# Performance work log

Measured on AMD Instinct MI355X. Metric: run time of the kernel, lower is better.

## Reference

```python
import jax, jax.numpy as jnp
import numpy as np

NUM_HEADS = 12
DIM_HEAD = 64
EPS = 1e-5


def _layer_norm(x, g, b):
    m = jnp.mean(x, axis=-1, keepdims=True)
    v = jnp.mean(jnp.square(x - m), axis=-1, keepdims=True)
    return (x - m) * jax.lax.rsqrt(v + EPS) * g + b


def setup_inputs() -> dict:
    key = jax.random.key(0)
    ks = jax.random.split(key, 3)
    B, S, L, D = 1, 128, 256, NUM_HEADS * DIM_HEAD
    x = jax.random.normal(ks[0], (B, S, L, D), dtype=jnp.float32)
    w_row = jax.random.normal(ks[1], (3 * D, D), dtype=jnp.float32) * 0.02
    b_row = jnp.zeros((3 * D,), dtype=jnp.float32)
    w_col = jax.random.normal(ks[2], (3 * D, D), dtype=jnp.float32) * 0.02
    b_col = jnp.zeros((3 * D,), dtype=jnp.float32)
    g1 = jnp.ones((D,), dtype=jnp.float32)
    beta1 = jnp.zeros((D,), dtype=jnp.float32)
    g2 = jnp.ones((D,), dtype=jnp.float32)
    beta2 = jnp.zeros((D,), dtype=jnp.float32)
    return {"x": x, "w_row": w_row, "b_row": b_row, "w_col": w_col,
            "b_col": b_col, "g1": g1, "beta1": beta1, "g2": g2, "beta2": beta2}


def reference(x, w_row, b_row, w_col, b_col, g1, beta1, g2, beta2):
    B, S, L, D = x.shape
    H, dh = NUM_HEADS, DIM_HEAD

    def qkv(inp, w, b):
        p = inp @ w.T + b                      # [B,S,L,3D]
        q, k, v = jnp.split(p, 3, axis=-1)
        rs = lambda t: t.reshape(B, S, L, H, dh)
        return rs(q), rs(k), rs(v)

    # --- tied row attention: logits summed over S (no 1/sqrt(dh) scaling, as in source) ---
    q, k, v = qkv(x, w_row, b_row)
    row_attn = jnp.einsum('bsihc,bsjhc->bhij', q, k)      # [B,H,L,L]
    row_attn = jax.nn.softmax(row_attn, axis=-1)
    row_out = jnp.einsum('bhij,bsjhd->bsihd', row_attn, v).reshape(B, S, L, D)
    out = _layer_norm(x + row_out, g1, beta1)

    # --- column attention: softmax over the j (sequence) axis ---
    q, k, v = qkv(out, w_col, b_col)
    col_attn = jnp.einsum('bilhc,bjlhc->bhijl', q, k)     # [B,H,S,S,L]
    col_attn = jax.nn.softmax(col_attn, axis=-2)
    col_out = jnp.einsum('bhijl,bjlhd->bilhd', col_attn, v).reshape(B, S, L, D)
    out = _layer_norm(out + col_out, g2, beta2)
    return out
```

## Files before the change

### kernel.cpp

```cpp
#include <hip/hip_runtime.h>

#define S_DIM 128
#define L_DIM 256
#define D_DIM 768
#define H_DIM 12
#define TD    2304
#define NROW  32768
#define KDIM  768
#define LN_EPS 1e-5f

typedef unsigned short u16;
typedef unsigned int   u32;
typedef _Float16 f16;
typedef _Float16 f16x8 __attribute__((ext_vector_type(8)));
typedef _Float16 f16x4 __attribute__((ext_vector_type(4)));
typedef float    f32x4 __attribute__((ext_vector_type(4)));

#define WS_QT_OFF     0
#define WS_KT_OFF     50331648
#define WS_VT_OFF     100663296
#define WS_P_OFF      0
#define WS_LPART_OFF  150994944
#define WS_PT_OFF     163577856
#define WS_XH_OFF     166723584
#define WS_WRH_OFF    217055232
#define WS_WCH_OFF    220594176

__device__ __forceinline__ float h2f(u16 v) {
    union { u16 u; f16 h; } c; c.u = v; return (float)c.h;
}

__device__ __forceinline__ void gload_lds16(const void* g, void* l) {
    __builtin_amdgcn_global_load_lds((const __attribute__((address_space(1))) void*)g,
                                     (__attribute__((address_space(3))) void*)l, 16, 0, 0);
}

__global__ __launch_bounds__(256)
void cvt_f32_f16(const float* __restrict__ in, f16* __restrict__ out)
{
    int i = blockIdx.x * 256 + threadIdx.x;
    float4 v = ((const float4*)in)[i];
    f16x4 o; o.x = (f16)v.x; o.y = (f16)v.y; o.z = (f16)v.z; o.w = (f16)v.w;
    ((f16x4*)out)[i] = o;
}

#define MFMA_PROLOG(KROW)                                                     \
    __shared__ f16 As[128 * 32];                                              \
    __shared__ f16 Bs[128 * 32];                                              \
    const int tid  = threadIdx.x;                                             \
    const int lane = tid & 63;                                                \
    const int w    = tid >> 6;                                                \
    const int wr   = (w >> 1) * 64;                                           \
    const int wc   = (w & 1) * 64;                                            \
    const int lm   = lane & 15;                                               \
    const int q    = lane >> 4;                                               \
    size_t soff[2];                                                           \
    int    ldsc[2];                                                           \
    _Pragma("unroll")                                                         \
    for (int t = 0; t < 2; ++t) {                                             \
        int c  = w * 128 + t * 64 + lane;                                     \
        int m  = c >> 2;                                                      \
        int gj = (c & 3) ^ ((m >> 1) & 3);                                    \
        soff[t] = (size_t)m * (KROW) + gj * 8;                                \
        ldsc[t] = (w * 128 + t * 64) * 8;                                     \
    }                                                                         \
    int chA[4], chB[4];                                                       \
    _Pragma("unroll")                                                         \
    for (int t = 0; t < 4; ++t) {                                             \
        int ma = wr + t * 16 + lm;                                            \
        chA[t] = ma * 4 + (q ^ ((ma >> 1) & 3));                              \
        int mb = wc + t * 16 + lm;                                            \
        chB[t] = mb * 4 + (q ^ ((mb >> 1) & 3));                              \
    }                                                                         \
    f32x4 acc[4][4];                                                          \
    _Pragma("unroll")                                                         \
    for (int i = 0; i < 4; ++i)                                               \
        _Pragma("unroll")                                                     \
        for (int j = 0; j < 4; ++j) acc[i][j] = (f32x4)0.f;

#define MFMA_KLOOP(baseA, baseB, KLEN)                                        \
    for (int k0 = 0; k0 < (KLEN); k0 += 32) {                                 \
        _Pragma("unroll")                                                     \
        for (int t = 0; t < 2; ++t) {                                         \
            gload_lds16((baseA) + soff[t] + k0, &As[ldsc[t]]);                \
            gload_lds16((baseB) + soff[t] + k0, &Bs[ldsc[t]]);                \
        }                                                                     \
        __syncthreads();                                                      \
        f16x8 af[4], bf[4];                                                   \
        _Pragma("unroll")                                                     \
        for (int t = 0; t < 4; ++t) af[t] = *(const f16x8*)&As[chA[t] * 8];   \
        _Pragma("unroll")                                                     \
        for (int t = 0; t < 4; ++t) bf[t] = *(const f16x8*)&Bs[chB[t] * 8];   \
        _Pragma("unroll")                                                     \
        for (int mt = 0; mt < 4; ++mt)                                        \
            _Pragma("unroll")                                                 \
            for (int nt = 0; nt < 4; ++nt)                                    \
                acc[mt][nt] = __builtin_amdgcn_mfma_f32_16x16x32_f16(         \
                    af[mt], bf[nt], acc[mt][nt], 0, 0, 0);                    \
        __syncthreads();                                                      \
    }

__global__ __launch_bounds__(256)
void mfma_gemm_qkv(const f16* __restrict__ A, const f16* __restrict__ W,
                   const float* __restrict__ bias, f16* __restrict__ C)
{
    const int row0 = blockIdx.y * 128;
    const int col0 = blockIdx.x * 128;
    MFMA_PROLOG(KDIM)
    const f16* baseA = A + (size_t)row0 * KDIM;
    const f16* baseB = W + (size_t)col0 * KDIM;
    MFMA_KLOOP(baseA, baseB, KDIM)

    float bv[4];
#pragma unroll
    for (int nt = 0; nt < 4; ++nt) bv[nt] = bias[col0 + wc + nt * 16 + lm];
#pragma unroll
    for (int mt = 0; mt < 4; ++mt) {
        int grow = row0 + wr + mt * 16 + q * 4;
#pragma unroll
        for (int nt = 0; nt < 4; ++nt) {
            int gcol = col0 + wc + nt * 16 + lm;
#pragma unroll
            for (int r = 0; r < 4; ++r)
                C[(size_t)(grow + r) * TD + gcol] = (f16)(acc[mt][nt][r] + bv[nt]);
        }
    }
}

__global__ __launch_bounds__(256)
void mfma_gemm_row(const f16* __restrict__ A, const f16* __restrict__ W,
                   const float* __restrict__ bias,
                   f16* __restrict__ qt, f16* __restrict__ kt,
                   f16* __restrict__ vt)
{
    const int row0 = blockIdx.y * 128;
    const int col0 = blockIdx.x * 128;
    MFMA_PROLOG(KDIM)
    const f16* baseA = A + (size_t)row0 * KDIM;
    const f16* baseB = W + (size_t)col0 * KDIM;
    MFMA_KLOOP(baseA, baseB, KDIM)

    if (col0 < 1536) {
        f16* dst = (col0 < 768) ? qt : kt;
        const int cbase = (col0 < 768) ? col0 : col0 - 768;
#pragma unroll
        for (int nt = 0; nt < 4; ++nt) {
            int gcol = cbase + wc + nt * 16 + lm;
            int h = gcol >> 6, c = gcol & 63;
            float b = bias[col0 + wc + nt * 16 + lm];
#pragma unroll
            for (int mt = 0; mt < 4; ++mt) {
                int n0 = row0 + wr + mt * 16 + q * 4;
#pragma unroll
                for (int r = 0; r < 4; ++r) {
                    int n = n0 + r;
                    int s = n >> 8, i = n & 255;
                    dst[(((size_t)h * 256 + i) * 128 + s) * 64 + c] =
                        (f16)(acc[mt][nt][r] + b);
                }
            }
        }
    } else {
#pragma unroll
        for (int nt = 0; nt < 4; ++nt) {
            int gcol = col0 + wc + nt * 16 + lm;
            int vcol = gcol - 1536;
            int h = vcol >> 6, d = vcol & 63;
            float b = bias[gcol];
#pragma unroll
            for (int mt = 0; mt < 4; ++mt) {
                int n0 = row0 + wr + mt * 16 + q * 4;
                int s = n0 >> 8, j0 = n0 & 255;
                f16x4 pack;
#pragma unroll
                for (int r = 0; r < 4; ++r) pack[r] = (f16)(acc[mt][nt][r] + b);
                *(f16x4*)&vt[((((size_t)h * 128 + s) * 64 + d) << 8) + j0] = pack;
            }
        }
    }
}

__global__ __launch_bounds__(256)
void row_logits_mfma(const f16* __restrict__ qt, const f16* __restrict__ kt,
                     float* __restrict__ lpart)
{
    const int i0 = blockIdx.y * 128;
    const int j0 = blockIdx.x * 128;
    const int h  = blockIdx.z >> 2;
    const int sp = blockIdx.z & 3;
    MFMA_PROLOG(8192)
    const f16* baseA = qt + ((size_t)h * 256 + i0) * 8192 + sp * 2048;
    const f16* baseB = kt + ((size_t)h * 256 + j0) * 8192 + sp * 2048;
    MFMA_KLOOP(baseA, baseB, 2048)

    float* outp = lpart + (size_t)(sp * 12 + h) * 65536;
#pragma unroll
    for (int mt = 0; mt < 4; ++mt) {
        int grow = i0 + wr + mt * 16 + q * 4;
#pragma unroll
        for (int nt = 0; nt < 4; ++nt) {
            int gcol = j0 + wc + nt * 16 + lm;
#pragma unroll
            for (int r = 0; r < 4; ++r)
                outp[(size_t)(grow + r) * 256 + gcol] = acc[mt][nt][r];
        }
    }
}

__global__ __launch_bounds__(256)
void softmax256_4(const float* __restrict__ lpart, f16* __restrict__ pt)
{
    __shared__ float red[256];
    const int t = threadIdx.x;
    const size_t idx = (size_t)blockIdx.x * 256 + t;
    const size_t P = (size_t)12 * 65536;
    float v = lpart[idx] + lpart[idx + P] + lpart[idx + 2*P] + lpart[idx + 3*P];
    red[t] = v; __syncthreads();
    for (int w = 128; w > 0; w >>= 1) { if (t < w) red[t] = fmaxf(red[t], red[t+w]); __syncthreads(); }
    float m = red[0];
    __syncthreads();
    float e = __expf(v - m);
    red[t] = e; __syncthreads();
    for (int w = 128; w > 0; w >>= 1) { if (t < w) red[t] += red[t+w]; __syncthreads(); }
    pt[idx] = (f16)(e / red[0]);
}

__global__ __launch_bounds__(256)
void row_pv_mfma(const f16* __restrict__ pt, const f16* __restrict__ vt,
                 float* __restrict__ rout)
{
    const int n0t = blockIdx.x * 128;
    const int i0  = blockIdx.y * 128;
    const int h   = blockIdx.z;
    MFMA_PROLOG(256)
    const f16* baseA = pt + (size_t)h * 65536 + (size_t)i0 * 256;
    const f16* baseB = vt + ((size_t)h * 8192 + n0t) * 256;
    MFMA_KLOOP(baseA, baseB, 256)

#pragma unroll
    for (int mt = 0; mt < 4; ++mt) {
        int irow = i0 + wr + mt * 16 + q * 4;
#pragma unroll
        for (int nt = 0; nt < 4; ++nt) {
            int n = n0t + wc + nt * 16 + lm;
            int s = n >> 6, d = n & 63;
#pragma unroll
            for (int r = 0; r < 4; ++r)
                rout[(size_t)(s * 256 + irow + r) * D_DIM + h * 64 + d] =
                    acc[mt][nt][r];
        }
    }
}

__global__ __launch_bounds__(256)
void add_ln_out16(const float* __restrict__ x, const float* __restrict__ r,
                  const float* __restrict__ g, const float* __restrict__ beta,
                  f16* __restrict__ out16)
{
    __shared__ float red[256];
    const int n = blockIdx.x, t = threadIdx.x;
    const float* xp = x + (size_t)n * D_DIM;
    const float* rp = r + (size_t)n * D_DIM;
    float v[3]; float s = 0.f;
#pragma unroll
    for (int e = 0; e < 3; ++e) { v[e] = xp[t + e*256] + rp[t + e*256]; s += v[e]; }
    red[t] = s; __syncthreads();
    for (int w = 128; w > 0; w >>= 1) { if (t < w) red[t] += red[t+w]; __syncthreads(); }
    float mean = red[0] * (1.f/768.f);
    __syncthreads();
    float sq = 0.f;
#pragma unroll
    for (int e = 0; e < 3; ++e) { float d = v[e] - mean; sq += d*d; }
    red[t] = sq; __syncthreads();
    for (int w = 128; w > 0; w >>= 1) { if (t < w) red[t] += red[t+w]; __syncthreads(); }
    float rstd = rsqrtf(red[0] * (1.f/768.f) + LN_EPS);
#pragma unroll
    for (int e = 0; e < 3; ++e) {
        int idx = t + e*256;
        out16[(size_t)n * D_DIM + idx] = (f16)((v[e] - mean) * rstd * g[idx] + beta[idx]);
    }
}

__global__ __launch_bounds__(256)
void add_ln_in16(const f16* __restrict__ x16, float* __restrict__ r,
                 const float* __restrict__ g, const float* __restrict__ beta)
{
    __shared__ float red[256];
    const int n = blockIdx.x, t = threadIdx.x;
    const f16*   xp = x16 + (size_t)n * D_DIM;
    float*       rp = r   + (size_t)n * D_DIM;
    float v[3]; float s = 0.f;
#pragma unroll
    for (int e = 0; e < 3; ++e) { v[e] = (float)xp[t + e*256] + rp[t + e*256]; s += v[e]; }
    red[t] = s; __syncthreads();
    for (int w = 128; w > 0; w >>= 1) { if (t < w) red[t] += red[t+w]; __syncthreads(); }
    float mean = red[0] * (1.f/768.f);
    __syncthreads();
    float sq = 0.f;
#pragma unroll
    for (int e = 0; e < 3; ++e) { float d = v[e] - mean; sq += d*d; }
    red[t] = sq; __syncthreads();
    for (int w = 128; w > 0; w >>= 1) { if (t < w) red[t] += red[t+w]; __syncthreads(); }
    float rstd = rsqrtf(red[0] * (1.f/768.f) + LN_EPS);
#pragma unroll
    for (int e = 0; e < 3; ++e) {
        int idx = t + e*256;
        rp[idx] = (v[e] - mean) * rstd * g[idx] + beta[idx];
    }
}

__global__ __launch_bounds__(256, 3)
void col_attn_mfma(const f16* __restrict__ p, float* __restrict__ cout)
{
    __shared__ char smem[54272];
    f16* Qs = (f16*)smem;
    f16* Ks = (f16*)(smem + 18432);
    f16* Ps = (f16*)smem;
    f16* Vt = (f16*)(smem + 36864);

    const int tid  = threadIdx.x;
    const int lane = tid & 63;
    const int w    = tid >> 6;
    const int lm   = lane & 15;
    const int q    = lane >> 4;
    const int l = blockIdx.x, h = blockIdx.y;
    const int ib = w * 32;

    {
        const int r  = tid >> 1;
        const int hc = (tid & 1) * 32;
        const f16* rowp = p + (size_t)(r * 256 + l) * TD + h * 64 + hc;
#pragma unroll
        for (int cc = 0; cc < 4; ++cc)
            *(float4*)&Qs[r * 72 + hc + cc * 8] = *(const float4*)(rowp + cc * 8);
#pragma unroll
        for (int cc = 0; cc < 4; ++cc)
            *(float4*)&Ks[r * 72 + hc + cc * 8] = *(const float4*)(rowp + 768 + cc * 8);
#pragma unroll
        for (int cc = 0; cc < 4; ++cc) {
            union { float4 f; u16 u[8]; } vb;
            vb.f = *(const float4*)(rowp + 1536 + cc * 8);
#pragma unroll
            for (int e = 0; e < 8; ++e) {
                int d = hc + cc * 8 + e;
                ((u16*)Vt)[d * 136 + r] = vb.u[e];
            }
        }
    }
    __syncthreads();

    f32x4 acc[2][8];
#pragma unroll
    for (int mt = 0; mt < 2; ++mt)
#pragma unroll
        for (int nt = 0; nt < 8; ++nt) acc[mt][nt] = (f32x4)0.f;
#pragma unroll
    for (int ks = 0; ks < 2; ++ks) {
        f16x8 af[2];
#pragma unroll
        for (int mt = 0; mt < 2; ++mt)
            af[mt] = *(const f16x8*)&Qs[(ib + mt * 16 + lm) * 72 + ks * 32 + q * 8];
#pragma unroll
        for (int nt = 0; nt < 8; ++nt) {
            f16x8 bf = *(const f16x8*)&Ks[(nt * 16 + lm) * 72 + ks * 32 + q * 8];
#pragma unroll
            for (int mt = 0; mt < 2; ++mt)
                acc[mt][nt] = __builtin_amdgcn_mfma_f32_16x16x32_f16(
                    af[mt], bf, acc[mt][nt], 0, 0, 0);
        }
    }
    __syncthreads();

    float inv_sum[2][4];
#pragma unroll
    for (int mt = 0; mt < 2; ++mt) {
#pragma unroll
        for (int r = 0; r < 4; ++r) {
            float m = acc[mt][0][r];
#pragma unroll
            for (int nt = 1; nt < 8; ++nt) m = fmaxf(m, acc[mt][nt][r]);
#pragma unroll
            for (int d = 1; d < 16; d <<= 1) m = fmaxf(m, __shfl_xor(m, d));
            float s = 0.f;
#pragma unroll
            for (int nt = 0; nt < 8; ++nt) {
                float e = __expf(acc[mt][nt][r] - m);
                acc[mt][nt][r] = e; s += e;
            }
#pragma unroll
            for (int d = 1; d < 16; d <<= 1) s += __shfl_xor(s, d);
            inv_sum[mt][r] = 1.f / s;
        }
        const int irow = ib + mt * 16 + q * 4;
#pragma unroll
        for (int nt = 0; nt < 8; ++nt) {
            const int jj = nt * 16 + lm;
#pragma unroll
            for (int r = 0; r < 4; ++r)
                Ps[(irow + r) * 136 + jj] = (f16)acc[mt][nt][r];
        }
    }
    __syncthreads();

    f32x4 acc2[2][4];
#pragma unroll
    for (int mt = 0; mt < 2; ++mt)
#pragma unroll
        for (int nt = 0; nt < 4; ++nt) acc2[mt][nt] = (f32x4)0.f;
#pragma unroll
    for (int ks = 0; ks < 4; ++ks) {
        f16x8 pf[2];
#pragma unroll
        for (int mt = 0; mt < 2; ++mt)
            pf[mt] = *(const f16x8*)&Ps[(ib + mt * 16 + lm) * 136 + ks * 32 + q * 8];
#pragma unroll
        for (int nt = 0; nt < 4; ++nt) {
            f16x8 vf = *(const f16x8*)&Vt[(nt * 16 + lm) * 136 + ks * 32 + q * 8];
#pragma unroll
            for (int mt = 0; mt < 2; ++mt)
                acc2[mt][nt] = __builtin_amdgcn_mfma_f32_16x16x32_f16(
                    pf[mt], vf, acc2[mt][nt], 0, 0, 0);
        }
    }

#pragma unroll
    for (int mt = 0; mt < 2; ++mt) {
        const int irow = ib + mt * 16 + q * 4;
#pragma unroll
        for (int nt = 0; nt < 4; ++nt) {
            const int d = nt * 16 + lm;
#pragma unroll
            for (int r = 0; r < 4; ++r)
                cout[(size_t)((irow + r) * 256 + l) * D_DIM + h * 64 + d] =
                    acc2[mt][nt][r] * inv_sum[mt][r];
        }
    }
}

extern "C" void kernel_launch(void* const* d_in, const int* in_sizes, int n_in,
                              void* d_out, int out_size, void* d_ws, size_t ws_size,
                              hipStream_t stream)
{
    const float* x     = (const float*)d_in[0];
    const float* w_row = (const float*)d_in[1];
    const float* b_row = (const float*)d_in[2];
    const float* w_col = (const float*)d_in[3];
    const float* b_col = (const float*)d_in[4];
    const float* g1    = (const float*)d_in[5];
    const float* be1   = (const float*)d_in[6];
    const float* g2    = (const float*)d_in[7];
    const float* be2   = (const float*)d_in[8];
    float* out = (float*)d_out;

    char* ws = (char*)d_ws;
    f16*   qt     = (f16*)(ws + WS_QT_OFF);
    f16*   kt     = (f16*)(ws + WS_KT_OFF);
    f16*   vt     = (f16*)(ws + WS_VT_OFF);
    f16*   p      = (f16*)(ws + WS_P_OFF);
    float* lpart  = (float*)(ws + WS_LPART_OFF);
    f16*   pt     = (f16*)(ws + WS_PT_OFF);
    f16*   xh     = (f16*)(ws + WS_XH_OFF);
    f16*   wrh    = (f16*)(ws + WS_WRH_OFF);
    f16*   wch    = (f16*)(ws + WS_WCH_OFF);

    cvt_f32_f16<<<NROW * D_DIM / 1024, 256, 0, stream>>>(x, xh);
    cvt_f32_f16<<<TD * D_DIM / 1024, 256, 0, stream>>>(w_row, wrh);
    cvt_f32_f16<<<TD * D_DIM / 1024, 256, 0, stream>>>(w_col, wch);
    mfma_gemm_row<<<dim3(TD/128, NROW/128), 256, 0, stream>>>(xh, wrh, b_row, qt, kt, vt);
    row_logits_mfma<<<dim3(2, 2, 48), 256, 0, stream>>>(qt, kt, lpart);
    softmax256_4<<<H_DIM * L_DIM, 256, 0, stream>>>(lpart, pt);
    row_pv_mfma<<<dim3(64, 2, H_DIM), 256, 0, stream>>>(pt, vt, out);
    add_ln_out16<<<NROW, 256, 0, stream>>>(x, out, g1, be1, xh);
    mfma_gemm_qkv<<<dim3(TD/128, NROW/128), 256, 0, stream>>>(xh, wch, b_col, p);
    col_attn_mfma<<<dim3(L_DIM, H_DIM), 256, 0, stream>>>(p, out);
    add_ln_in16<<<NROW, 256, 0, stream>>>(xh, out, g2, be2);
}
```

Measured before the change: 737.4 us.

## Use 256x256 double-buffered MFMA tiles with XOR LDS swizzle and grid remap for QKV GEMMs

Replaces the 128x128 single-buffered GEMM tile with a 256x256 tile computed by 512 threads. The K loop uses two LDS buffers so the next K slice loads while the current one computes. LDS reads use an XOR-swizzled layout, and the block index is remapped so neighbouring blocks share A and B tiles in cache. s_setprio is raised around the MFMA bursts. The aim is higher operand reuse, fewer bank conflicts and hidden load latency in the two large projection GEMMs. The cost is higher register and LDS use (128KB of LDS per block), which may limit occupancy.

```diff
diff --git a/kernel.cpp b/kernel.cpp
--- a/kernel.cpp
+++ b/kernel.cpp
@@ -100,22 +100,101 @@
         __syncthreads();                                                      \
     }
 
-__global__ __launch_bounds__(256)
+#define G256_PROLOG(KROW)                                                     \
+    __shared__ f16 As0[256 * 64];                                             \
+    __shared__ f16 Bs0[256 * 64];                                             \
+    __shared__ f16 As1[256 * 64];                                             \
+    __shared__ f16 Bs1[256 * 64];                                             \
+    const int tid  = threadIdx.x;                                             \
+    const int lane = tid & 63;                                                \
+    const int w    = tid >> 6;                                                \
+    const int wr   = (w >> 2) * 128;                                          \
+    const int wc   = (w & 3) * 64;                                            \
+    const int lm   = lane & 15;                                               \
+    const int q    = lane >> 4;                                               \
+    size_t soff[4];                                                           \
+    int    ldsb[4];                                                           \
+    _Pragma("unroll")                                                         \
+    for (int i = 0; i < 4; ++i) {                                             \
+        int c = i * 512 + tid;                                                \
+        int r = c >> 3;                                                       \
+        int j = (c & 7) ^ (r & 7);                                            \
+        soff[i] = (size_t)r * (KROW) + j * 8;                                 \
+        ldsb[i] = (i * 512 + w * 64) * 8;                                     \
+    }                                                                         \
+    f32x4 acc[8][4];                                                          \
+    _Pragma("unroll")                                                         \
+    for (int i = 0; i < 8; ++i)                                               \
+        _Pragma("unroll")                                                     \
+        for (int j = 0; j < 4; ++j) acc[i][j] = (f32x4)0.f;
+
+#define G256_STAGE(Ad, Bd, baseA, baseB, kk)                                  \
+    _Pragma("unroll")                                                         \
+    for (int i = 0; i < 4; ++i) {                                             \
+        gload_lds16((baseA) + soff[i] + (kk) * 64, &Ad[ldsb[i]]);             \
+        gload_lds16((baseB) + soff[i] + (kk) * 64, &Bd[ldsb[i]]);             \
+    }
+
+#define G256_FRAG(buf, row, ks)                                               \
+    (*(const f16x8*)&buf[(size_t)(row) * 64 +                                 \
+                         ((((ks) * 4 + q) ^ ((row) & 7)) * 8)])
+
+#define G256_COMPUTE(Ab, Bb)                                                  \
+    _Pragma("unroll")                                                         \
+    for (int ks = 0; ks < 2; ++ks) {                                          \
+        f16x8 af[8], bf[4];                                                   \
+        _Pragma("unroll")                                                     \
+        for (int mt = 0; mt < 8; ++mt)                                        \
+            af[mt] = G256_FRAG(Ab, wr + mt * 16 + lm, ks);                    \
+        _Pragma("unroll")                                                     \
+        for (int nt = 0; nt < 4; ++nt)                                        \
+            bf[nt] = G256_FRAG(Bb, wc + nt * 16 + lm, ks);                    \
+        __builtin_amdgcn_s_setprio(1);                                        \
+        _Pragma("unroll")                                                     \
+        for (int mt = 0; mt < 8; ++mt)                                        \
+            _Pragma("unroll")                                                 \
+            for (int nt = 0; nt < 4; ++nt)                                    \
+                acc[mt][nt] = __builtin_amdgcn_mfma_f32_16x16x32_f16(         \
+                    af[mt], bf[nt], acc[mt][nt], 0, 0, 0);                    \
+        __builtin_amdgcn_s_setprio(0);                                        \
+    }
+
+#define G256_KLOOP(baseA, baseB, KLEN)                                        \
+    G256_STAGE(As0, Bs0, baseA, baseB, 0)                                     \
+    __syncthreads();                                                          \
+    _Pragma("clang loop unroll(disable)")                                     \
+    for (int kk = 0; kk < (KLEN) / 64; kk += 2) {                             \
+        G256_STAGE(As1, Bs1, baseA, baseB, kk + 1)                            \
+        G256_COMPUTE(As0, Bs0)                                                \
+        __syncthreads();                                                      \
+        if (kk + 2 < (KLEN) / 64) {                                           \
+            G256_STAGE(As0, Bs0, baseA, baseB, kk + 2)                        \
+        }                                                                     \
+        G256_COMPUTE(As1, Bs1)                                                \
+        __syncthreads();                                                      \
+    }
+
+#define G256_SWIZZLE()                                                        \
+    const int wg   = blockIdx.y * 9 + blockIdx.x;                             \
+    const int swz  = (wg & 7) * 144 + (wg >> 3);                              \
+    const int row0 = (swz / 9) * 256;                                         \
+    const int col0 = (swz % 9) * 256;
+
+__global__ __launch_bounds__(512, 2)
 void mfma_gemm_qkv(const f16* __restrict__ A, const f16* __restrict__ W,
                    const float* __restrict__ bias, f16* __restrict__ C)
 {
-    const int row0 = blockIdx.y * 128;
-    const int col0 = blockIdx.x * 128;
-    MFMA_PROLOG(KDIM)
+    G256_SWIZZLE()
+    G256_PROLOG(KDIM)
     const f16* baseA = A + (size_t)row0 * KDIM;
     const f16* baseB = W + (size_t)col0 * KDIM;
-    MFMA_KLOOP(baseA, baseB, KDIM)
+    G256_KLOOP(baseA, baseB, KDIM)
 
     float bv[4];
 #pragma unroll
     for (int nt = 0; nt < 4; ++nt) bv[nt] = bias[col0 + wc + nt * 16 + lm];
 #pragma unroll
-    for (int mt = 0; mt < 4; ++mt) {
+    for (int mt = 0; mt < 8; ++mt) {
         int grow = row0 + wr + mt * 16 + q * 4;
 #pragma unroll
         for (int nt = 0; nt < 4; ++nt) {
@@ -127,18 +206,17 @@
     }
 }
 
-__global__ __launch_bounds__(256)
+__global__ __launch_bounds__(512, 2)
 void mfma_gemm_row(const f16* __restrict__ A, const f16* __restrict__ W,
                    const float* __restrict__ bias,
                    f16* __restrict__ qt, f16* __restrict__ kt,
                    f16* __restrict__ vt)
 {
-    const int row0 = blockIdx.y * 128;
-    const int col0 = blockIdx.x * 128;
-    MFMA_PROLOG(KDIM)
+    G256_SWIZZLE()
+    G256_PROLOG(KDIM)
     const f16* baseA = A + (size_t)row0 * KDIM;
     const f16* baseB = W + (size_t)col0 * KDIM;
-    MFMA_KLOOP(baseA, baseB, KDIM)
+    G256_KLOOP(baseA, baseB, KDIM)
 
     if (col0 < 1536) {
         f16* dst = (col0 < 768) ? qt : kt;
@@ -149,13 +227,13 @@
             int h = gcol >> 6, c = gcol & 63;
             float b = bias[col0 + wc + nt * 16 + lm];
 #pragma unroll
-            for (int mt = 0; mt < 4; ++mt) {
+            for (int mt = 0; mt < 8; ++mt) {
                 int n0 = row0 + wr + mt * 16 + q * 4;
 #pragma unroll
                 for (int r = 0; r < 4; ++r) {
                     int n = n0 + r;
-                    int s = n >> 8, i = n & 255;
-                    dst[(((size_t)h * 256 + i) * 128 + s) * 64 + c] =
+                    int s = n >> 8, ii = n & 255;
+                    dst[(((size_t)h * 256 + ii) * 128 + s) * 64 + c] =
                         (f16)(acc[mt][nt][r] + b);
                 }
             }
@@ -168,7 +246,7 @@
             int h = vcol >> 6, d = vcol & 63;
             float b = bias[gcol];
 #pragma unroll
-            for (int mt = 0; mt < 4; ++mt) {
+            for (int mt = 0; mt < 8; ++mt) {
                 int n0 = row0 + wr + mt * 16 + q * 4;
                 int s = n0 >> 8, j0 = n0 & 255;
                 f16x4 pack;
@@ -466,12 +544,12 @@
     cvt_f32_f16<<<NROW * D_DIM / 1024, 256, 0, stream>>>(x, xh);
     cvt_f32_f16<<<TD * D_DIM / 1024, 256, 0, stream>>>(w_row, wrh);
     cvt_f32_f16<<<TD * D_DIM / 1024, 256, 0, stream>>>(w_col, wch);
-    mfma_gemm_row<<<dim3(TD/128, NROW/128), 256, 0, stream>>>(xh, wrh, b_row, qt, kt, vt);
+    mfma_gemm_row<<<dim3(9, 128), 512, 0, stream>>>(xh, wrh, b_row, qt, kt, vt);
     row_logits_mfma<<<dim3(2, 2, 48), 256, 0, stream>>>(qt, kt, lpart);
     softmax256_4<<<H_DIM * L_DIM, 256, 0, stream>>>(lpart, pt);
     row_pv_mfma<<<dim3(64, 2, H_DIM), 256, 0, stream>>>(pt, vt, out);
     add_ln_out16<<<NROW, 256, 0, stream>>>(x, out, g1, be1, xh);
-    mfma_gemm_qkv<<<dim3(TD/128, NROW/128), 256, 0, stream>>>(xh, wch, b_col, p);
+    mfma_gemm_qkv<<<dim3(9, 128), 512, 0, stream>>>(xh, wch, b_col, p);
     col_attn_mfma<<<dim3(L_DIM, H_DIM), 256, 0, stream>>>(p, out);
     add_ln_in16<<<NROW, 256, 0, stream>>>(xh, out, g2, be2);
 }
```

Measured after the change: 839.0 us. 1.14x slower.

## Rewrite QKV GEMMs with 256x192 tiles, multi-buffered async LDS pipeline and swizzle

Applied to the files above, without the earlier changes.

Both QKV projection GEMMs now use 512-thread blocks computing 256x192 tiles with BK=64. The K loop is fully unrolled, with triple-buffered A and double-buffered B loaded straight into LDS through global_load_lds, explicit vmcnt waits, and a single barrier per stage. The LDS layout is XOR-swizzled to avoid bank conflicts, and the workgroup index is remapped so that neighbouring blocks share operand tiles in L2. The aim is to cut load stalls and synchronisation overhead in the two dominant GEMMs, at the cost of much higher LDS use (about 160 KB per block) and more register pressure.

```diff
diff --git a/kernel.cpp b/kernel.cpp
--- a/kernel.cpp
+++ b/kernel.cpp
@@ -25,10 +25,6 @@
 #define WS_XH_OFF     166723584
 #define WS_WRH_OFF    217055232
 #define WS_WCH_OFF    220594176
-
-__device__ __forceinline__ float h2f(u16 v) {
-    union { u16 u; f16 h; } c; c.u = v; return (float)c.h;
-}
 
 __device__ __forceinline__ void gload_lds16(const void* g, void* l) {
     __builtin_amdgcn_global_load_lds((const __attribute__((address_space(1))) void*)g,
@@ -100,25 +96,129 @@
         __syncthreads();                                                      \
     }
 
-__global__ __launch_bounds__(256)
+#define R3_WAIT_(N) asm volatile("s_waitcnt vmcnt(" #N ")" ::: "memory")
+#define R3_WAIT(N)  R3_WAIT_(N)
+
+#define R3_PROLOG()                                                           \
+    __shared__ f16 As0[256 * 64];                                             \
+    __shared__ f16 As1[256 * 64];                                             \
+    __shared__ f16 As2[256 * 64];                                             \
+    __shared__ f16 Bs0[192 * 64];                                             \
+    __shared__ f16 Bs1[192 * 64];                                             \
+    const int tid  = threadIdx.x;                                             \
+    const int lane = tid & 63;                                                \
+    const int w    = tid >> 6;                                                \
+    const int wr   = (w >> 1) * 64;                                           \
+    const int wc   = (w & 1) * 96;                                            \
+    const int lm   = lane & 15;                                               \
+    const int q    = lane >> 4;                                               \
+    size_t soffA[4];                                                          \
+    _Pragma("unroll")                                                         \
+    for (int i = 0; i < 4; ++i) {                                             \
+        int c = i * 512 + tid;                                                \
+        int r = c >> 3;                                                       \
+        int j = (c & 7) ^ (r & 7);                                            \
+        soffA[i] = (size_t)r * KDIM + j * 8;                                  \
+    }                                                                         \
+    size_t soffB[3];                                                          \
+    _Pragma("unroll")                                                         \
+    for (int i = 0; i < 3; ++i) {                                             \
+        int c = i * 512 + tid;                                                \
+        int r = c >> 3;                                                       \
+        int j = (c & 7) ^ (r & 7);                                            \
+        soffB[i] = (size_t)r * KDIM + j * 8;                                  \
+    }                                                                         \
+    f32x4 acc[4][6];                                                          \
+    _Pragma("unroll")                                                         \
+    for (int i = 0; i < 4; ++i)                                               \
+        _Pragma("unroll")                                                     \
+        for (int j = 0; j < 6; ++j) acc[i][j] = (f32x4)0.f;
+
+#define R3_STAGE_A(Ad, kk)                                                    \
+    _Pragma("unroll")                                                         \
+    for (int i = 0; i < 4; ++i)                                               \
+        gload_lds16(baseA + soffA[i] + (size_t)(kk) * 64,                     \
+                    &Ad[(i * 512 + w * 64) * 8]);
+
+#define R3_STAGE_B(Bd, kk)                                                    \
+    _Pragma("unroll")                                                         \
+    for (int i = 0; i < 3; ++i)                                               \
+        gload_lds16(baseB + soffB[i] + (size_t)(kk) * 64,                     \
+                    &Bd[(i * 512 + w * 64) * 8]);
+
+#define R3_FRAG(buf, row, ks)                                                 \
+    (*(const f16x8*)&buf[(size_t)(row) * 64 +                                 \
+                         ((((ks) * 4 + q) ^ ((row) & 7)) * 8)])
+
+#define R3_COMPUTE(Ab, Bb)                                                    \
+    _Pragma("unroll")                                                         \
+    for (int ks = 0; ks < 2; ++ks) {                                          \
+        f16x8 af[4], bf[6];                                                   \
+        _Pragma("unroll")                                                     \
+        for (int mt = 0; mt < 4; ++mt)                                        \
+            af[mt] = R3_FRAG(Ab, wr + mt * 16 + lm, ks);                      \
+        _Pragma("unroll")                                                     \
+        for (int nt = 0; nt < 6; ++nt)                                        \
+            bf[nt] = R3_FRAG(Bb, wc + nt * 16 + lm, ks);                      \
+        __builtin_amdgcn_s_setprio(1);                                        \
+        _Pragma("unroll")                                                     \
+        for (int mt = 0; mt < 4; ++mt)                                        \
+            _Pragma("unroll")                                                 \
+            for (int nt = 0; nt < 6; ++nt)                                    \
+                acc[mt][nt] = __builtin_amdgcn_mfma_f32_16x16x32_f16(         \
+                    af[mt], bf[nt], acc[mt][nt], 0, 0, 0);                    \
+        __builtin_amdgcn_s_setprio(0);                                        \
+    }
+
+#define R3_TILE(Ab, Bb, SB, Bn, kb, SA, An, ka, WN)                           \
+    R3_WAIT(WN);                                                              \
+    __builtin_amdgcn_s_barrier();                                             \
+    __builtin_amdgcn_sched_barrier(0);                                        \
+    if (SB) { R3_STAGE_B(Bn, kb) }                                            \
+    if (SA) { R3_STAGE_A(An, ka) }                                            \
+    R3_COMPUTE(Ab, Bb)
+
+#define R3_KLOOP768()                                                         \
+    R3_STAGE_A(As0, 0)                                                        \
+    R3_STAGE_B(Bs0, 0)                                                        \
+    R3_STAGE_A(As1, 1)                                                        \
+    R3_TILE(As0, Bs0, 1, Bs1, 1,  1, As2, 2,  4)                              \
+    R3_TILE(As1, Bs1, 1, Bs0, 2,  1, As0, 3,  4)                              \
+    R3_TILE(As2, Bs0, 1, Bs1, 3,  1, As1, 4,  4)                              \
+    R3_TILE(As0, Bs1, 1, Bs0, 4,  1, As2, 5,  4)                              \
+    R3_TILE(As1, Bs0, 1, Bs1, 5,  1, As0, 6,  4)                              \
+    R3_TILE(As2, Bs1, 1, Bs0, 6,  1, As1, 7,  4)                              \
+    R3_TILE(As0, Bs0, 1, Bs1, 7,  1, As2, 8,  4)                              \
+    R3_TILE(As1, Bs1, 1, Bs0, 8,  1, As0, 9,  4)                              \
+    R3_TILE(As2, Bs0, 1, Bs1, 9,  1, As1, 10, 4)                              \
+    R3_TILE(As0, Bs1, 1, Bs0, 10, 1, As2, 11, 4)                              \
+    R3_TILE(As1, Bs0, 1, Bs1, 11, 0, As0, 0,  4)                              \
+    R3_TILE(As2, Bs1, 0, Bs0, 0,  0, As0, 0,  0)
+
+#define R3_SWIZZLE()                                                          \
+    const int wg   = blockIdx.y * 12 + blockIdx.x;                            \
+    const int swz  = (wg & 7) * 192 + (wg >> 3);                              \
+    const int row0 = (swz / 12) * 256;                                        \
+    const int col0 = (swz % 12) * 192;
+
+__global__ __launch_bounds__(512, 2)
 void mfma_gemm_qkv(const f16* __restrict__ A, const f16* __restrict__ W,
                    const float* __restrict__ bias, f16* __restrict__ C)
 {
-    const int row0 = blockIdx.y * 128;
-    const int col0 = blockIdx.x * 128;
-    MFMA_PROLOG(KDIM)
+    R3_SWIZZLE()
+    R3_PROLOG()
     const f16* baseA = A + (size_t)row0 * KDIM;
     const f16* baseB = W + (size_t)col0 * KDIM;
-    MFMA_KLOOP(baseA, baseB, KDIM)
-
-    float bv[4];
-#pragma unroll
-    for (int nt = 0; nt < 4; ++nt) bv[nt] = bias[col0 + wc + nt * 16 + lm];
+    R3_KLOOP768()
+
+    float bv[6];
+#pragma unroll
+    for (int nt = 0; nt < 6; ++nt) bv[nt] = bias[col0 + wc + nt * 16 + lm];
 #pragma unroll
     for (int mt = 0; mt < 4; ++mt) {
         int grow = row0 + wr + mt * 16 + q * 4;
 #pragma unroll
-        for (int nt = 0; nt < 4; ++nt) {
+        for (int nt = 0; nt < 6; ++nt) {
             int gcol = col0 + wc + nt * 16 + lm;
 #pragma unroll
             for (int r = 0; r < 4; ++r)
@@ -127,24 +227,23 @@
     }
 }
 
-__global__ __launch_bounds__(256)
+__global__ __launch_bounds__(512, 2)
 void mfma_gemm_row(const f16* __restrict__ A, const f16* __restrict__ W,
                    const float* __restrict__ bias,
                    f16* __restrict__ qt, f16* __restrict__ kt,
                    f16* __restrict__ vt)
 {
-    const int row0 = blockIdx.y * 128;
-    const int col0 = blockIdx.x * 128;
-    MFMA_PROLOG(KDIM)
+    R3_SWIZZLE()
+    R3_PROLOG()
     const f16* baseA = A + (size_t)row0 * KDIM;
     const f16* baseB = W + (size_t)col0 * KDIM;
-    MFMA_KLOOP(baseA, baseB, KDIM)
+    R3_KLOOP768()
 
     if (col0 < 1536) {
         f16* dst = (col0 < 768) ? qt : kt;
         const int cbase = (col0 < 768) ? col0 : col0 - 768;
 #pragma unroll
-        for (int nt = 0; nt < 4; ++nt) {
+        for (int nt = 0; nt < 6; ++nt) {
             int gcol = cbase + wc + nt * 16 + lm;
             int h = gcol >> 6, c = gcol & 63;
             float b = bias[col0 + wc + nt * 16 + lm];
@@ -154,15 +253,15 @@
 #pragma unroll
                 for (int r = 0; r < 4; ++r) {
                     int n = n0 + r;
-                    int s = n >> 8, i = n & 255;
-                    dst[(((size_t)h * 256 + i) * 128 + s) * 64 + c] =
+                    int s = n >> 8, ii = n & 255;
+                    dst[(((size_t)h * 256 + ii) * 128 + s) * 64 + c] =
                         (f16)(acc[mt][nt][r] + b);
                 }
             }
         }
     } else {
 #pragma unroll
-        for (int nt = 0; nt < 4; ++nt) {
+        for (int nt = 0; nt < 6; ++nt) {
             int gcol = col0 + wc + nt * 16 + lm;
             int vcol = gcol - 1536;
             int h = vcol >> 6, d = vcol & 63;
@@ -466,12 +565,12 @@
     cvt_f32_f16<<<NROW * D_DIM / 1024, 256, 0, stream>>>(x, xh);
     cvt_f32_f16<<<TD * D_DIM / 1024, 256, 0, stream>>>(w_row, wrh);
     cvt_f32_f16<<<TD * D_DIM / 1024, 256, 0, stream>>>(w_col, wch);
-    mfma_gemm_row<<<dim3(TD/128, NROW/128), 256, 0, stream>>>(xh, wrh, b_row, qt, kt, vt);
+    mfma_gemm_row<<<dim3(12, 128), 512, 0, stream>>>(xh, wrh, b_row, qt, kt, vt);
     row_logits_mfma<<<dim3(2, 2, 48), 256, 0, stream>>>(qt, kt, lpart);
     softmax256_4<<<H_DIM * L_DIM, 256, 0, stream>>>(lpart, pt);
     row_pv_mfma<<<dim3(64, 2, H_DIM), 256, 0, stream>>>(pt, vt, out);
     add_ln_out16<<<NROW, 256, 0, stream>>>(x, out, g1, be1, xh);
-    mfma_gemm_qkv<<<dim3(TD/128, NROW/128), 256, 0, stream>>>(xh, wch, b_col, p);
+    mfma_gemm_qkv<<<dim3(12, 128), 512, 0, stream>>>(xh, wch, b_col, p);
     col_attn_mfma<<<dim3(L_DIM, H_DIM), 256, 0, stream>>>(p, out);
     add_ln_in16<<<NROW, 256, 0, stream>>>(xh, out, g2, be2);
 }
```

Result: no change. 725.2 us (-1.7%).

## Double-buffer QKV GEMMs with swizzled LDS, staged epilogues, and fp16 row output

Applied to the files above, without the earlier changes.

Rewrites both QKV projection GEMMs with a double-buffered 64-wide K pipeline that issues async global-to-LDS loads ahead of compute, uses XOR-swizzled LDS to avoid bank conflicts, and raises MFMA priority. Block order is remapped so neighbouring blocks share cache. Epilogues now stage through LDS so global stores to q/k/v and the output are coalesced 16-byte writes. Row-attention output is stored in fp16 in reused workspace, and the first layernorm reads the fp16 copy of x. That halves its traffic at some precision cost in the residual.

```diff
diff --git a/kernel.cpp b/kernel.cpp
--- a/kernel.cpp
+++ b/kernel.cpp
@@ -25,10 +25,6 @@
 #define WS_XH_OFF     166723584
 #define WS_WRH_OFF    217055232
 #define WS_WCH_OFF    220594176
-
-__device__ __forceinline__ float h2f(u16 v) {
-    union { u16 u; f16 h; } c; c.u = v; return (float)c.h;
-}
 
 __device__ __forceinline__ void gload_lds16(const void* g, void* l) {
     __builtin_amdgcn_global_load_lds((const __attribute__((address_space(1))) void*)g,
@@ -100,81 +96,198 @@
         __syncthreads();                                                      \
     }
 
-__global__ __launch_bounds__(256)
+#define R5_WAIT_(N) asm volatile("s_waitcnt vmcnt(" #N ")" ::: "memory")
+#define R5_WAIT(N)  R5_WAIT_(N)
+
+#define R5_PROLOG()                                                           \
+    __shared__ __align__(16) char SMEM[65536];                                \
+    f16* const As0 = (f16*)(SMEM);                                            \
+    f16* const Bs0 = (f16*)(SMEM + 16384);                                    \
+    f16* const As1 = (f16*)(SMEM + 32768);                                    \
+    f16* const Bs1 = (f16*)(SMEM + 49152);                                    \
+    const int tid  = threadIdx.x;                                             \
+    const int lane = tid & 63;                                                \
+    const int w    = tid >> 6;                                                \
+    const int wr   = (w >> 1) * 64;                                           \
+    const int wc   = (w & 1) * 64;                                            \
+    const int lm   = lane & 15;                                               \
+    const int q    = lane >> 4;                                               \
+    size_t soff[4];                                                           \
+    int    ldsb[4];                                                           \
+    _Pragma("unroll")                                                         \
+    for (int i = 0; i < 4; ++i) {                                             \
+        int c = i * 256 + tid;                                                \
+        int r = c >> 3;                                                       \
+        int j = (c & 7) ^ (r & 7);                                            \
+        soff[i] = (size_t)r * KDIM + j * 8;                                   \
+        ldsb[i] = (i * 256 + w * 64) * 8;                                     \
+    }                                                                         \
+    f32x4 acc[4][4];                                                          \
+    _Pragma("unroll")                                                         \
+    for (int i = 0; i < 4; ++i)                                               \
+        _Pragma("unroll")                                                     \
+        for (int j = 0; j < 4; ++j) acc[i][j] = (f32x4)0.f;
+
+#define R5_STAGE(Ad, Bd, kk)                                                  \
+    _Pragma("unroll")                                                         \
+    for (int i = 0; i < 4; ++i)                                               \
+        gload_lds16(baseA + soff[i] + (size_t)(kk) * 64, &Ad[ldsb[i]]);       \
+    _Pragma("unroll")                                                         \
+    for (int i = 0; i < 4; ++i)                                               \
+        gload_lds16(baseB + soff[i] + (size_t)(kk) * 64, &Bd[ldsb[i]]);
+
+#define R5_FRAG(buf, row, ks)                                                 \
+    (*(const f16x8*)&buf[(size_t)(row) * 64 +                                 \
+                         ((((ks) * 4 + q) ^ ((row) & 7)) * 8)])
+
+#define R5_COMPUTE(Ab, Bb)                                                    \
+    _Pragma("unroll")                                                         \
+    for (int ks = 0; ks < 2; ++ks) {                                          \
+        f16x8 af[4], bf[4];                                                   \
+        _Pragma("unroll")                                                     \
+        for (int mt = 0; mt < 4; ++mt)                                        \
+            af[mt] = R5_FRAG(Ab, wr + mt * 16 + lm, ks);                      \
+        _Pragma("unroll")                                                     \
+        for (int nt = 0; nt < 4; ++nt)                                        \
+            bf[nt] = R5_FRAG(Bb, wc + nt * 16 + lm, ks);                      \
+        __builtin_amdgcn_s_setprio(1);                                        \
+        _Pragma("unroll")                                                     \
+        for (int mt = 0; mt < 4; ++mt)                                        \
+            _Pragma("unroll")                                                 \
+            for (int nt = 0; nt < 4; ++nt)                                    \
+                acc[mt][nt] = __builtin_amdgcn_mfma_f32_16x16x32_f16(         \
+                    af[mt], bf[nt], acc[mt][nt], 0, 0, 0);                    \
+        __builtin_amdgcn_s_setprio(0);                                        \
+    }
+
+#define R5_TILE(Ac, Bc, An, Bn, kn, PF, WN)                                   \
+    if (PF) { R5_STAGE(An, Bn, kn) }                                          \
+    R5_WAIT(WN);                                                              \
+    __builtin_amdgcn_s_barrier();                                             \
+    __builtin_amdgcn_sched_barrier(0);                                        \
+    R5_COMPUTE(Ac, Bc)                                                        \
+    __builtin_amdgcn_sched_barrier(0);                                        \
+    __builtin_amdgcn_s_barrier();
+
+#define R5_KLOOP768()                                                         \
+    R5_STAGE(As0, Bs0, 0)                                                     \
+    R5_TILE(As0, Bs0, As1, Bs1, 1,  1, 8)                                     \
+    R5_TILE(As1, Bs1, As0, Bs0, 2,  1, 8)                                     \
+    R5_TILE(As0, Bs0, As1, Bs1, 3,  1, 8)                                     \
+    R5_TILE(As1, Bs1, As0, Bs0, 4,  1, 8)                                     \
+    R5_TILE(As0, Bs0, As1, Bs1, 5,  1, 8)                                     \
+    R5_TILE(As1, Bs1, As0, Bs0, 6,  1, 8)                                     \
+    R5_TILE(As0, Bs0, As1, Bs1, 7,  1, 8)                                     \
+    R5_TILE(As1, Bs1, As0, Bs0, 8,  1, 8)                                     \
+    R5_TILE(As0, Bs0, As1, Bs1, 9,  1, 8)                                     \
+    R5_TILE(As1, Bs1, As0, Bs0, 10, 1, 8)                                     \
+    R5_TILE(As0, Bs0, As1, Bs1, 11, 1, 8)                                     \
+    R5_TILE(As1, Bs1, As0, Bs0, 0,  0, 0)
+
+#define R5_SWIZZLE()                                                          \
+    const int wg   = blockIdx.y * 18 + blockIdx.x;                            \
+    const int swz  = (wg & 7) * 576 + (wg >> 3);                              \
+    const int row0 = (swz / 18) * 128;                                        \
+    const int col0 = (swz % 18) * 128;
+
+#define R5_DEPOSIT_ROWMAJOR(EP)                                               \
+    _Pragma("unroll")                                                         \
+    for (int mt = 0; mt < 4; ++mt)                                            \
+        _Pragma("unroll")                                                     \
+        for (int nt = 0; nt < 4; ++nt) {                                      \
+            const int col = wc + nt * 16 + lm;                                \
+            _Pragma("unroll")                                                 \
+            for (int r = 0; r < 4; ++r) {                                     \
+                const int n = wr + mt * 16 + q * 4 + r;                       \
+                EP[n * 128 + (((col >> 3) ^ (n & 7)) << 3) + (col & 7)] =     \
+                    (f16)(acc[mt][nt][r] + bv[nt]);                           \
+            }                                                                 \
+        }                                                                     \
+    __syncthreads();
+
+__global__ __launch_bounds__(256, 2)
 void mfma_gemm_qkv(const f16* __restrict__ A, const f16* __restrict__ W,
                    const float* __restrict__ bias, f16* __restrict__ C)
 {
-    const int row0 = blockIdx.y * 128;
-    const int col0 = blockIdx.x * 128;
-    MFMA_PROLOG(KDIM)
+    R5_SWIZZLE()
+    R5_PROLOG()
     const f16* baseA = A + (size_t)row0 * KDIM;
     const f16* baseB = W + (size_t)col0 * KDIM;
-    MFMA_KLOOP(baseA, baseB, KDIM)
+    R5_KLOOP768()
 
     float bv[4];
 #pragma unroll
     for (int nt = 0; nt < 4; ++nt) bv[nt] = bias[col0 + wc + nt * 16 + lm];
-#pragma unroll
-    for (int mt = 0; mt < 4; ++mt) {
-        int grow = row0 + wr + mt * 16 + q * 4;
-#pragma unroll
-        for (int nt = 0; nt < 4; ++nt) {
-            int gcol = col0 + wc + nt * 16 + lm;
-#pragma unroll
-            for (int r = 0; r < 4; ++r)
-                C[(size_t)(grow + r) * TD + gcol] = (f16)(acc[mt][nt][r] + bv[nt]);
-        }
-    }
-}
-
-__global__ __launch_bounds__(256)
+    f16* const EP = (f16*)SMEM;
+    R5_DEPOSIT_ROWMAJOR(EP)
+
+    {
+        const int n = tid >> 1, half = tid & 1;
+        f16* dst = C + (size_t)(row0 + n) * TD + col0 + half * 64;
+#pragma unroll
+        for (int c = 0; c < 8; ++c) {
+            const int ch = half * 8 + c;
+            float4 v4 = *(const float4*)&EP[n * 128 + ((ch ^ (n & 7)) << 3)];
+            *(float4*)(dst + c * 8) = v4;
+        }
+    }
+}
+
+__global__ __launch_bounds__(256, 2)
 void mfma_gemm_row(const f16* __restrict__ A, const f16* __restrict__ W,
                    const float* __restrict__ bias,
                    f16* __restrict__ qt, f16* __restrict__ kt,
                    f16* __restrict__ vt)
 {
-    const int row0 = blockIdx.y * 128;
-    const int col0 = blockIdx.x * 128;
-    MFMA_PROLOG(KDIM)
+    R5_SWIZZLE()
+    R5_PROLOG()
     const f16* baseA = A + (size_t)row0 * KDIM;
     const f16* baseB = W + (size_t)col0 * KDIM;
-    MFMA_KLOOP(baseA, baseB, KDIM)
+    R5_KLOOP768()
+
+    float bv[4];
+#pragma unroll
+    for (int nt = 0; nt < 4; ++nt) bv[nt] = bias[col0 + wc + nt * 16 + lm];
+    const int s     = row0 >> 8;
+    const int ibase = row0 & 255;
 
     if (col0 < 1536) {
-        f16* dst = (col0 < 768) ? qt : kt;
-        const int cbase = (col0 < 768) ? col0 : col0 - 768;
-#pragma unroll
-        for (int nt = 0; nt < 4; ++nt) {
-            int gcol = cbase + wc + nt * 16 + lm;
-            int h = gcol >> 6, c = gcol & 63;
-            float b = bias[col0 + wc + nt * 16 + lm];
-#pragma unroll
-            for (int mt = 0; mt < 4; ++mt) {
-                int n0 = row0 + wr + mt * 16 + q * 4;
+        f16* const EP = (f16*)SMEM;
+        R5_DEPOSIT_ROWMAJOR(EP)
+        const int n  = tid & 127, hb = tid >> 7;
+        const int gcol = ((col0 < 768) ? col0 : col0 - 768) + hb * 64;
+        const int h  = gcol >> 6;
+        f16* dst = ((col0 < 768) ? qt : kt) +
+                   ((((size_t)h * 256 + ibase + n) * 128 + s) << 6);
+#pragma unroll
+        for (int c = 0; c < 8; ++c) {
+            const int ch = hb * 8 + c;
+            float4 v4 = *(const float4*)&EP[n * 128 + ((ch ^ (n & 7)) << 3)];
+            *(float4*)(dst + c * 8) = v4;
+        }
+    } else {
+        f16* const EPT = (f16*)SMEM;
+#pragma unroll
+        for (int mt = 0; mt < 4; ++mt)
+#pragma unroll
+            for (int nt = 0; nt < 4; ++nt) {
+                const int lc = wc + nt * 16 + lm;
 #pragma unroll
                 for (int r = 0; r < 4; ++r) {
-                    int n = n0 + r;
-                    int s = n >> 8, i = n & 255;
-                    dst[(((size_t)h * 256 + i) * 128 + s) * 64 + c] =
-                        (f16)(acc[mt][nt][r] + b);
+                    const int n = wr + mt * 16 + q * 4 + r;
+                    EPT[lc * 136 + n] = (f16)(acc[mt][nt][r] + bv[nt]);
                 }
             }
-        }
-    } else {
-#pragma unroll
-        for (int nt = 0; nt < 4; ++nt) {
-            int gcol = col0 + wc + nt * 16 + lm;
-            int vcol = gcol - 1536;
-            int h = vcol >> 6, d = vcol & 63;
-            float b = bias[gcol];
-#pragma unroll
-            for (int mt = 0; mt < 4; ++mt) {
-                int n0 = row0 + wr + mt * 16 + q * 4;
-                int s = n0 >> 8, j0 = n0 & 255;
-                f16x4 pack;
-#pragma unroll
-                for (int r = 0; r < 4; ++r) pack[r] = (f16)(acc[mt][nt][r] + b);
-                *(f16x4*)&vt[((((size_t)h * 128 + s) * 64 + d) << 8) + j0] = pack;
+        __syncthreads();
+        if (tid < 128) {
+            const int lc = tid;
+            const int vcol = col0 - 1536 + lc;
+            const int h = vcol >> 6, d = vcol & 63;
+            f16* dst = vt + ((((size_t)h * 128 + s) * 64 + d) << 8) + ibase;
+#pragma unroll
+            for (int c = 0; c < 16; ++c) {
+                float4 v4 = *(const float4*)&EPT[lc * 136 + c * 8];
+                *(float4*)(dst + c * 8) = v4;
             }
         }
     }
@@ -227,7 +340,7 @@
 
 __global__ __launch_bounds__(256)
 void row_pv_mfma(const f16* __restrict__ pt, const f16* __restrict__ vt,
-                 float* __restrict__ rout)
+                 f16* __restrict__ rout)
 {
     const int n0t = blockIdx.x * 128;
     const int i0  = blockIdx.y * 128;
@@ -247,23 +360,23 @@
 #pragma unroll
             for (int r = 0; r < 4; ++r)
                 rout[(size_t)(s * 256 + irow + r) * D_DIM + h * 64 + d] =
-                    acc[mt][nt][r];
+                    (f16)acc[mt][nt][r];
         }
     }
 }
 
 __global__ __launch_bounds__(256)
-void add_ln_out16(const float* __restrict__ x, const float* __restrict__ r,
+void add_ln_out16(const f16* __restrict__ x16, const f16* __restrict__ r,
                   const float* __restrict__ g, const float* __restrict__ beta,
                   f16* __restrict__ out16)
 {
     __shared__ float red[256];
     const int n = blockIdx.x, t = threadIdx.x;
-    const float* xp = x + (size_t)n * D_DIM;
-    const float* rp = r + (size_t)n * D_DIM;
+    const f16* xp = x16 + (size_t)n * D_DIM;
+    const f16* rp = r   + (size_t)n * D_DIM;
     float v[3]; float s = 0.f;
 #pragma unroll
-    for (int e = 0; e < 3; ++e) { v[e] = xp[t + e*256] + rp[t + e*256]; s += v[e]; }
+    for (int e = 0; e < 3; ++e) { v[e] = (float)xp[t + e*256] + (float)rp[t + e*256]; s += v[e]; }
     red[t] = s; __syncthreads();
     for (int w = 128; w > 0; w >>= 1) { if (t < w) red[t] += red[t+w]; __syncthreads(); }
     float mean = red[0] * (1.f/768.f);
@@ -462,16 +575,17 @@
     f16*   xh     = (f16*)(ws + WS_XH_OFF);
     f16*   wrh    = (f16*)(ws + WS_WRH_OFF);
     f16*   wch    = (f16*)(ws + WS_WCH_OFF);
+    f16*   rout_h = qt;
 
     cvt_f32_f16<<<NROW * D_DIM / 1024, 256, 0, stream>>>(x, xh);
     cvt_f32_f16<<<TD * D_DIM / 1024, 256, 0, stream>>>(w_row, wrh);
     cvt_f32_f16<<<TD * D_DIM / 1024, 256, 0, stream>>>(w_col, wch);
-    mfma_gemm_row<<<dim3(TD/128, NROW/128), 256, 0, stream>>>(xh, wrh, b_row, qt, kt, vt);
+    mfma_gemm_row<<<dim3(18, 256), 256, 0, stream>>>(xh, wrh, b_row, qt, kt, vt);
     row_logits_mfma<<<dim3(2, 2, 48), 256, 0, stream>>>(qt, kt, lpart);
     softmax256_4<<<H_DIM * L_DIM, 256, 0, stream>>>(lpart, pt);
-    row_pv_mfma<<<dim3(64, 2, H_DIM), 256, 0, stream>>>(pt, vt, out);
-    add_ln_out16<<<NROW, 256, 0, stream>>>(x, out, g1, be1, xh);
-    mfma_gemm_qkv<<<dim3(TD/128, NROW/128), 256, 0, stream>>>(xh, wch, b_col, p);
+    row_pv_mfma<<<dim3(64, 2, H_DIM), 256, 0, stream>>>(pt, vt, rout_h);
+    add_ln_out16<<<NROW, 256, 0, stream>>>(xh, rout_h, g1, be1, xh);
+    mfma_gemm_qkv<<<dim3(18, 256), 256, 0, stream>>>(xh, wch, b_col, p);
     col_attn_mfma<<<dim3(L_DIM, H_DIM), 256, 0, stream>>>(p, out);
     add_ln_in16<<<NROW, 256, 0, stream>>>(xh, out, g2, be2);
 }
```

After: 759.5 us. +3.0%, slower.
